# Optimization experiments

Measured on AMD Instinct MI355X. Metric: run time of the kernel, lower is better.

## Reference

```python
import jax, jax.numpy as jnp
import numpy as np

EPS = 1e-12  # matches torch F.normalize eps clamp


def _l2norm(v, axis):
    n = jnp.sqrt(jnp.sum(v * v, axis=axis, keepdims=True))
    return v / jnp.maximum(n, EPS)


def setup_inputs() -> dict:
    key = jax.random.key(0)
    k1, k2, k3, k4 = jax.random.split(key, 4)
    N, C, H, W, K = 64, 128, 64, 64, 64
    x = jax.random.normal(k1, (N, C, H, W), dtype=jnp.float32)
    conv_w = jax.random.normal(k2, (K, C), dtype=jnp.float32) * 0.1  # 1x1 conv weight squeezed
    conv_b = jax.random.normal(k3, (K,), dtype=jnp.float32) * 0.1
    centroids = jax.random.uniform(k4, (K, C), dtype=jnp.float32)
    return {"x": x, "conv_w": conv_w, "conv_b": conv_b, "centroids": centroids}


def reference(x, conv_w, conv_b, centroids):
    N, C = x.shape[:2]
    K = centroids.shape[0]
    xf = x.reshape(N, C, -1)                                   # (N, C, P) with P = H*W
    # 1x1 conv == per-pixel linear map over channels
    logits = jnp.einsum('ncp,kc->nkp', xf, conv_w) + conv_b[None, :, None]
    a = jax.nn.softmax(logits, axis=1)                         # soft assignment over clusters
    # vlad[n,k,c] = sum_p a[n,k,p] * (x[n,c,p] - centroids[k,c])
    vlad = jnp.einsum('nkp,ncp->nkc', a, xf) \
        - jnp.sum(a, axis=-1)[:, :, None] * centroids[None]    # (N, K, C)
    vlad = _l2norm(vlad, axis=2)                               # intra-cluster normalization
    vlad = vlad.reshape(N, K * C)
    return _l2norm(vlad, axis=1)
```

## Files before the change

kernel.cpp:

```cpp
#include <hip/hip_runtime.h>
#include <math.h>

#define NNIMG 64
#define CCH 128
#define KK 64
#define PP 4096
#define BSPLIT 16
#define PB 256
#define PC 32
#define NCHUNK (PB / PC)

typedef __attribute__((ext_vector_type(8))) short short8;
typedef __attribute__((ext_vector_type(4))) float f32x4;

__device__ __forceinline__ unsigned short bf16_rtne(float f) {
  unsigned u = __float_as_uint(f);
  unsigned r = u + 0x7FFFu + ((u >> 16) & 1u);
  return (unsigned short)(r >> 16);
}
__device__ __forceinline__ float bf16_tof(unsigned short h) {
  return __uint_as_float(((unsigned)h) << 16);
}
__device__ __forceinline__ void lgkm_barrier() {
  __asm__ volatile("s_waitcnt lgkmcnt(0)\n\ts_barrier" ::: "memory");
}

__global__ __launch_bounds__(128, 2) void netvlad_main(
    const float* __restrict__ x, const float* __restrict__ conv_w,
    const float* __restrict__ conv_b, const float* __restrict__ centroids,
    float* __restrict__ out) {
  __shared__ __align__(16) unsigned int pc[2][PC * 66];
  __shared__ __align__(16) unsigned short a_lds[KK * 40];
  __shared__ float asum_buf[2 * KK];

  const int t = threadIdx.x;
  const int lane = t & 63;
  const int wv = t >> 6;
  const int m = lane & 15;
  const int q = lane >> 4;

  const int n = blockIdx.x >> 4;
  const int blk = blockIdx.x & 15;
  const float* xbase = x + (size_t)n * CCH * PP + blk * PB;

  const int lrow = lane >> 3;
  const int lpx = (lane & 7) * 4;
  f32x4 sreg[8];
  auto issue_loads = [&](int ch) {
#pragma unroll
    for (int j = 0; j < 8; ++j) {
      const int row = wv * 64 + (j >> 1) * 16 + lrow * 2 + (j & 1);
      sreg[j] = *(const f32x4*)(xbase + (size_t)row * PP + ch * PC + lpx);
    }
  };

  issue_loads(0);

  short8 Whi[4][4];
#pragma unroll
  for (int kt = 0; kt < 4; ++kt)
#pragma unroll
    for (int cs = 0; cs < 4; ++cs) {
      const float* wp = conv_w + (kt * 16 + m) * CCH + cs * 32 + q * 8;
      float4 wa = *(const float4*)wp;
      float4 wb = *(const float4*)(wp + 4);
      float fv[8] = {wa.x, wa.y, wa.z, wa.w, wb.x, wb.y, wb.z, wb.w};
      short8 h;
#pragma unroll
      for (int j = 0; j < 8; ++j) h[j] = (short)bf16_rtne(fv[j]);
      Whi[kt][cs] = h;
    }
  float b_regs[4][4];
#pragma unroll
  for (int kt = 0; kt < 4; ++kt)
#pragma unroll
    for (int r = 0; r < 4; ++r) b_regs[kt][r] = conv_b[kt * 16 + q * 4 + r];

  f32x4 vacc[4][4];
#pragma unroll
  for (int kt = 0; kt < 4; ++kt)
#pragma unroll
    for (int ct = 0; ct < 4; ++ct) vacc[kt][ct] = (f32x4){0.f, 0.f, 0.f, 0.f};
  float asum_acc[16];
#pragma unroll
  for (int i = 0; i < 16; ++i) asum_acc[i] = 0.f;

  const int prow = wv * 16 + m;
  const unsigned sel_hi = 0x07060302u;
  const unsigned sel_g2 = (m & 1) ? 0x07060302u : 0x05040100u;

#pragma unroll 1
  for (int ch = 0; ch < NCHUNK; ++ch) {
    unsigned int* pcb = pc[ch & 1];

#pragma unroll
    for (int u = 0; u < 4; ++u) {
      const int e = wv * 32 + u * 8 + lrow;
      f32x4 ev = sreg[2 * u];
      f32x4 od = sreg[2 * u + 1];
#pragma unroll
      for (int pi = 0; pi < 4; ++pi)
        pcb[(lpx + pi) * 66 + e] =
            __builtin_amdgcn_perm(__float_as_uint(od[pi]), __float_as_uint(ev[pi]), sel_hi);
    }
    if (ch + 1 < NCHUNK) issue_loads(ch + 1);
    lgkm_barrier();

    f32x4 acc1[4];
#pragma unroll
    for (int kt = 0; kt < 4; ++kt)
      acc1[kt] = (f32x4){b_regs[kt][0], b_regs[kt][1], b_regs[kt][2], b_regs[kt][3]};
    const unsigned int* pcrow = pcb + prow * 66;
#pragma unroll
    for (int cs = 0; cs < 4; ++cs) {
      uint2 u01 = *(const uint2*)&pcrow[16 * cs + 4 * q];
      uint2 u23 = *(const uint2*)&pcrow[16 * cs + 4 * q + 2];
      unsigned hs[4] = {u01.x, u01.y, u23.x, u23.y};
      short8 Bf;
      __builtin_memcpy(&Bf, hs, 16);
#pragma unroll
      for (int kt = 0; kt < 4; ++kt)
        acc1[kt] = __builtin_amdgcn_mfma_f32_16x16x32_bf16(Whi[kt][cs], Bf, acc1[kt], 0, 0, 0);
    }

    float ssum = 0.f;
#pragma unroll
    for (int kt = 0; kt < 4; ++kt)
#pragma unroll
      for (int r = 0; r < 4; ++r) {
        float e = __expf(acc1[kt][r]);
        acc1[kt][r] = e;
        ssum += e;
      }
    ssum += __shfl_xor(ssum, 16, 64);
    ssum += __shfl_xor(ssum, 32, 64);
    float inv = 1.0f / ssum;
#pragma unroll
    for (int kt = 0; kt < 4; ++kt)
#pragma unroll
      for (int r = 0; r < 4; ++r) {
        float a = acc1[kt][r] * inv;
        unsigned short h = bf16_rtne(a);
        asum_acc[kt * 4 + r] += bf16_tof(h);
        a_lds[(kt * 16 + q * 4 + r) * 40 + prow] = h;
      }
    lgkm_barrier();

    short8 Af[4];
#pragma unroll
    for (int kt = 0; kt < 4; ++kt)
      Af[kt] = *(const short8*)&a_lds[(kt * 16 + m) * 40 + q * 8];
#pragma unroll
    for (int ct = 0; ct < 4; ++ct) {
      const int ebase = wv * 32 + ct * 8 + (m >> 1);
      unsigned g[8];
#pragma unroll
      for (int j = 0; j < 8; ++j) g[j] = pcb[(q * 8 + j) * 66 + ebase];
      unsigned hs2[4];
#pragma unroll
      for (int i = 0; i < 4; ++i)
        hs2[i] = __builtin_amdgcn_perm(g[2 * i + 1], g[2 * i], sel_g2);
      short8 Bf;
      __builtin_memcpy(&Bf, hs2, 16);
#pragma unroll
      for (int kt = 0; kt < 4; ++kt)
        vacc[kt][ct] = __builtin_amdgcn_mfma_f32_16x16x32_bf16(Af[kt], Bf, vacc[kt][ct], 0, 0, 0);
    }
  }

#pragma unroll
  for (int i = 0; i < 16; ++i) {
    float v = asum_acc[i];
    v += __shfl_xor(v, 1, 64);
    v += __shfl_xor(v, 2, 64);
    v += __shfl_xor(v, 4, 64);
    v += __shfl_xor(v, 8, 64);
    if (m == 0) asum_buf[wv * 64 + (i >> 2) * 16 + q * 4 + (i & 3)] = v;
  }
  lgkm_barrier();
  float s_k[16];
#pragma unroll
  for (int i = 0; i < 16; ++i) {
    const int k = (i >> 2) * 16 + q * 4 + (i & 3);
    s_k[i] = asum_buf[k] + asum_buf[KK + k];
  }
  float* orow = out + (size_t)n * (KK * CCH);
#pragma unroll
  for (int kt = 0; kt < 4; ++kt)
#pragma unroll
    for (int ct = 0; ct < 4; ++ct)
#pragma unroll
      for (int r = 0; r < 4; ++r) {
        const int k = kt * 16 + q * 4 + r;
        const int c = wv * 64 + ct * 16 + m;
        const float v = vacc[kt][ct][r] - s_k[kt * 4 + r] * centroids[k * CCH + c];
        atomicAdd(&orow[k * CCH + c], v);
      }
}

__global__ __launch_bounds__(256) void netvlad_norm(float* __restrict__ out) {
  const int t = threadIdx.x;
  const int w = t >> 6, ln = t & 63;
  const int idx = blockIdx.x * 4 + w;
  float* vr = out + (size_t)idx * CCH;
  const int c = ln * 2;
  float2 v = *(const float2*)&vr[c];
  float ssq = v.x * v.x + v.y * v.y;
#pragma unroll
  for (int off = 32; off > 0; off >>= 1) ssq += __shfl_xor(ssq, off, 64);
  float inv = 0.125f / fmaxf(sqrtf(ssq), 1e-12f);
  float2 o;
  o.x = v.x * inv;
  o.y = v.y * inv;
  *(float2*)&vr[c] = o;
}

extern "C" void kernel_launch(void* const* d_in, const int* in_sizes, int n_in,
                              void* d_out, int out_size, void* d_ws, size_t ws_size,
                              hipStream_t stream) {
  const float* x = (const float*)d_in[0];
  const float* conv_w = (const float*)d_in[1];
  const float* conv_b = (const float*)d_in[2];
  const float* centroids = (const float*)d_in[3];
  float* out = (float*)d_out;

  (void)d_ws;
  (void)ws_size;

  hipMemsetAsync(d_out, 0, (size_t)NNIMG * KK * CCH * sizeof(float), stream);
  netvlad_main<<<NNIMG * BSPLIT, 128, 0, stream>>>(x, conv_w, conv_b, centroids, out);
  netvlad_norm<<<NNIMG * KK / 4, 256, 0, stream>>>(out);
}
```

Baseline: 242.4 us.

## Replace atomic reduction with workspace partials and a fused finish-normalize kernel

```diff
diff --git a/kernel.cpp b/kernel.cpp
--- a/kernel.cpp
+++ b/kernel.cpp
@@ -5,8 +5,8 @@
 #define CCH 128
 #define KK 64
 #define PP 4096
-#define BSPLIT 16
-#define PB 256
+#define BSPLIT 32
+#define PB (PP / BSPLIT)
 #define PC 32
 #define NCHUNK (PB / PC)
 
@@ -25,10 +25,11 @@
   __asm__ volatile("s_waitcnt lgkmcnt(0)\n\ts_barrier" ::: "memory");
 }
 
+template <bool USE_WS>
 __global__ __launch_bounds__(128, 2) void netvlad_main(
     const float* __restrict__ x, const float* __restrict__ conv_w,
     const float* __restrict__ conv_b, const float* __restrict__ centroids,
-    float* __restrict__ out) {
+    float* __restrict__ vout, float* __restrict__ aout) {
   __shared__ __align__(16) unsigned int pc[2][PC * 66];
   __shared__ __align__(16) unsigned short a_lds[KK * 40];
   __shared__ float asum_buf[2 * KK];
@@ -39,8 +40,8 @@
   const int m = lane & 15;
   const int q = lane >> 4;
 
-  const int n = blockIdx.x >> 4;
-  const int blk = blockIdx.x & 15;
+  const int n = blockIdx.x / BSPLIT;
+  const int blk = blockIdx.x % BSPLIT;
   const float* xbase = x + (size_t)n * CCH * PP + blk * PB;
 
   const int lrow = lane >> 3;
@@ -178,24 +179,69 @@
     if (m == 0) asum_buf[wv * 64 + (i >> 2) * 16 + q * 4 + (i & 3)] = v;
   }
   lgkm_barrier();
-  float s_k[16];
-#pragma unroll
-  for (int i = 0; i < 16; ++i) {
-    const int k = (i >> 2) * 16 + q * 4 + (i & 3);
-    s_k[i] = asum_buf[k] + asum_buf[KK + k];
-  }
-  float* orow = out + (size_t)n * (KK * CCH);
-#pragma unroll
-  for (int kt = 0; kt < 4; ++kt)
-#pragma unroll
-    for (int ct = 0; ct < 4; ++ct)
-#pragma unroll
-      for (int r = 0; r < 4; ++r) {
-        const int k = kt * 16 + q * 4 + r;
-        const int c = wv * 64 + ct * 16 + m;
-        const float v = vacc[kt][ct][r] - s_k[kt * 4 + r] * centroids[k * CCH + c];
-        atomicAdd(&orow[k * CCH + c], v);
-      }
+
+  if (USE_WS) {
+    float* vrow = vout + (size_t)blockIdx.x * (KK * CCH);
+#pragma unroll
+    for (int kt = 0; kt < 4; ++kt)
+#pragma unroll
+      for (int ct = 0; ct < 4; ++ct)
+#pragma unroll
+        for (int r = 0; r < 4; ++r) {
+          const int idx = (kt * 16 + q * 4 + r) * CCH + wv * 64 + ct * 16 + m;
+          vrow[idx] = vacc[kt][ct][r];
+        }
+    if (t < KK) aout[blockIdx.x * KK + t] = asum_buf[t] + asum_buf[KK + t];
+  } else {
+    float s_k[16];
+#pragma unroll
+    for (int i = 0; i < 16; ++i) {
+      const int k = (i >> 2) * 16 + q * 4 + (i & 3);
+      s_k[i] = asum_buf[k] + asum_buf[KK + k];
+    }
+    float* orow = vout + (size_t)n * (KK * CCH);
+#pragma unroll
+    for (int kt = 0; kt < 4; ++kt)
+#pragma unroll
+      for (int ct = 0; ct < 4; ++ct)
+#pragma unroll
+        for (int r = 0; r < 4; ++r) {
+          const int k = kt * 16 + q * 4 + r;
+          const int c = wv * 64 + ct * 16 + m;
+          atomicAdd(&orow[k * CCH + c],
+                    vacc[kt][ct][r] - s_k[kt * 4 + r] * centroids[k * CCH + c]);
+        }
+  }
+}
+
+__global__ __launch_bounds__(256) void netvlad_finish_ws(
+    const float* __restrict__ vp, const float* __restrict__ agp,
+    const float* __restrict__ centroids, float* __restrict__ out) {
+  const int t = threadIdx.x;
+  const int w = t >> 6, ln = t & 63;
+  const int idx = blockIdx.x * 4 + w;
+  const int n = idx >> 6, k = idx & 63;
+  const int c = ln * 2;
+  float a0 = 0.f, a1 = 0.f, s = 0.f;
+#pragma unroll
+  for (int b = 0; b < BSPLIT; ++b) {
+    const float* vr = vp + (size_t)(n * BSPLIT + b) * (KK * CCH) + k * CCH + c;
+    float2 v = *(const float2*)vr;
+    a0 += v.x;
+    a1 += v.y;
+    s += agp[(n * BSPLIT + b) * KK + k];
+  }
+  float2 ce = *(const float2*)&centroids[k * CCH + c];
+  float v0 = a0 - s * ce.x;
+  float v1 = a1 - s * ce.y;
+  float ssq = v0 * v0 + v1 * v1;
+#pragma unroll
+  for (int off = 32; off > 0; off >>= 1) ssq += __shfl_xor(ssq, off, 64);
+  float inv = 0.125f / fmaxf(sqrtf(ssq), 1e-12f);
+  float2 o;
+  o.x = v0 * inv;
+  o.y = v1 * inv;
+  *(float2*)&out[(size_t)n * (KK * CCH) + k * CCH + c] = o;
 }
 
 __global__ __launch_bounds__(256) void netvlad_norm(float* __restrict__ out) {
@@ -224,10 +270,19 @@
   const float* centroids = (const float*)d_in[3];
   float* out = (float*)d_out;
 
-  (void)d_ws;
-  (void)ws_size;
-
-  hipMemsetAsync(d_out, 0, (size_t)NNIMG * KK * CCH * sizeof(float), stream);
-  netvlad_main<<<NNIMG * BSPLIT, 128, 0, stream>>>(x, conv_w, conv_b, centroids, out);
-  netvlad_norm<<<NNIMG * KK / 4, 256, 0, stream>>>(out);
-}
+  const size_t WS_NEEDED =
+      ((size_t)NNIMG * BSPLIT * KK * CCH + (size_t)NNIMG * BSPLIT * KK) * sizeof(float);
+
+  if (ws_size >= WS_NEEDED) {
+    float* vp = (float*)d_ws;
+    float* agp = vp + (size_t)NNIMG * BSPLIT * KK * CCH;
+    netvlad_main<true><<<NNIMG * BSPLIT, 128, 0, stream>>>(x, conv_w, conv_b,
+                                                           centroids, vp, agp);
+    netvlad_finish_ws<<<NNIMG * KK / 4, 256, 0, stream>>>(vp, agp, centroids, out);
+  } else {
+    hipMemsetAsync(d_out, 0, (size_t)NNIMG * KK * CCH * sizeof(float), stream);
+    netvlad_main<false><<<NNIMG * BSPLIT, 128, 0, stream>>>(x, conv_w, conv_b,
+                                                            centroids, out, nullptr);
+    netvlad_norm<<<NNIMG * KK / 4, 256, 0, stream>>>(out);
+  }
+}
```

Result: faster. 226.9 us (-6.4%).
